# Optimization experiments

Hardware: AMD Instinct MI355X
Metric: run time of the kernel (lower is better)

The kernel has to match this reference:

```python
import jax, jax.numpy as jnp
import numpy as np

LN_EPS = 1e-6

def layernorm(x, w, b):
    m = jnp.mean(x, axis=-1, keepdims=True)
    v = jnp.mean((x - m) ** 2, axis=-1, keepdims=True)
    return (x - m) * jax.lax.rsqrt(v + LN_EPS) * w + b

def rotate_half(x):
    x1, x2 = jnp.split(x, 2, axis=-1)
    return jnp.concatenate([-x2, x1], axis=-1)

def headwise_lowrank(x, U, V, b):
    # x: [B,S,D], U: [H,D,r], V: [H,r,hd] -> [B,S,H*hd]
    xu = jnp.einsum('bsd,hdr->bshr', x, U)
    y = jnp.einsum('bshr,hre->bshe', xu, V)
    B, S, H, E = y.shape
    return y.reshape(B, S, H * E) + b

def setup_inputs() -> dict:
    key = jax.random.key(0)
    B, S, D, H, HD = 4, 2048, 768, 12, 64
    RA, RF, DFF = 32, 512, 3072
    ks = jax.random.split(key, 20)
    s = 0.02
    inp = {
        'x': jax.random.normal(ks[0], (B, S, D), jnp.float32),
        'attn_norm_w': jnp.ones((D,), jnp.float32),
        'attn_norm_b': jnp.zeros((D,), jnp.float32),
        'Uq': jax.random.normal(ks[1], (H, D, RA), jnp.float32) * s,
        'Vq': jax.random.normal(ks[2], (H, RA, HD), jnp.float32),
        'bq': jax.random.normal(ks[3], (D,), jnp.float32) * s,
        'Uk': jax.random.normal(ks[4], (H, D, RA), jnp.float32) * s,
        'Vk': jax.random.normal(ks[5], (H, RA, HD), jnp.float32),
        'bk': jax.random.normal(ks[6], (D,), jnp.float32) * s,
        'Uv': jax.random.normal(ks[7], (H, D, RA), jnp.float32) * s,
        'Vv': jax.random.normal(ks[8], (H, RA, HD), jnp.float32),
        'bv': jax.random.normal(ks[9], (D,), jnp.float32) * s,
        'Wo_w': jax.random.normal(ks[10], (D, D), jnp.float32) * s,
        'Wo_b': jax.random.normal(ks[11], (D,), jnp.float32) * s,
        'mlp_norm_w': jnp.ones((D,), jnp.float32),
        'mlp_norm_b': jnp.zeros((D,), jnp.float32),
        'Ui': jax.random.normal(ks[12], (D, RF), jnp.float32) * s,
        'Vi': jax.random.normal(ks[13], (RF, 2 * DFF), jnp.float32),
        'bi': jax.random.normal(ks[14], (2 * DFF,), jnp.float32) * s,
        'Uo': jax.random.normal(ks[15], (DFF, RF), jnp.float32) * s,
        'Vo': jax.random.normal(ks[16], (RF, D), jnp.float32),
        'bo': jax.random.normal(ks[17], (D,), jnp.float32) * s,
    }
    # real RoPE tables [S, HD]
    inv_freq = 1.0 / (10000.0 ** (np.arange(0, HD, 2, dtype=np.float32) / HD))
    t = np.arange(S, dtype=np.float32)
    freqs = np.outer(t, inv_freq)  # [S, HD/2]
    emb = np.concatenate([freqs, freqs], axis=-1)
    inp['cos'] = jnp.asarray(np.cos(emb))
    inp['sin'] = jnp.asarray(np.sin(emb))
    return inp

def reference(x, attn_norm_w, attn_norm_b, Uq, Vq, bq, Uk, Vk, bk, Uv, Vv, bv,
              cos, sin, Wo_w, Wo_b, mlp_norm_w, mlp_norm_b, Ui, Vi, bi, Uo, Vo, bo):
    B, S, D = x.shape
    H, HD = Vq.shape[0], Vq.shape[2]
    # --- attention sub-block (pre-norm) ---
    h = layernorm(x, attn_norm_w, attn_norm_b)
    q = headwise_lowrank(h, Uq, Vq, bq).reshape(B, S, H, HD).transpose(0, 2, 1, 3)
    k = headwise_lowrank(h, Uk, Vk, bk).reshape(B, S, H, HD).transpose(0, 2, 1, 3)
    v = headwise_lowrank(h, Uv, Vv, bv).reshape(B, S, H, HD).transpose(0, 2, 1, 3)
    c = cos[None, None]  # [1,1,S,HD]
    s_ = sin[None, None]
    q = q * c + rotate_half(q) * s_
    k = k * c + rotate_half(k) * s_
    scale = 1.0 / jnp.sqrt(jnp.asarray(HD, q.dtype))
    scores = jnp.einsum('bhqd,bhkd->bhqk', q, k) * scale
    attn = jax.nn.softmax(scores, axis=-1)
    o = jnp.einsum('bhqk,bhkd->bhqd', attn, v)
    o = o.transpose(0, 2, 1, 3).reshape(B, S, D)
    x1 = x + o @ Wo_w.T + Wo_b
    # --- FFN sub-block (pre-norm, low-rank GEGLU) ---
    h2 = layernorm(x1, mlp_norm_w, mlp_norm_b)
    u = (h2 @ Ui) @ Vi + bi  # [B,S,2*dff]
    g1, g2 = jnp.split(u, 2, axis=-1)
    g = jax.nn.gelu(g1, approximate=True) * g2
    y = (g @ Uo) @ Vo + bo
    return x1 + y
```

## Files before the change

kernel.cpp:

```cpp
#include <hip/hip_runtime.h>
#include <hip/hip_bf16.h>
#include <math.h>

#define NTOK 8192
#define SEQ  2048
#define DM   768
#define NH   12
#define HD2  64
#define RA   32
#define NG   3072

typedef __attribute__((ext_vector_type(8))) short bf16x8;
typedef __attribute__((ext_vector_type(4))) float f32x4;

__device__ __forceinline__ float b2f(unsigned short u) {
    union { unsigned int i; float f; } v; v.i = ((unsigned int)u) << 16; return v.f;
}
__device__ __forceinline__ unsigned short f2b_rne(float f) {
    union { float f; unsigned int i; } v; v.f = f;
    unsigned int b = v.i + 0x7FFFu + ((v.i >> 16) & 1u);
    return (unsigned short)(b >> 16);
}
__device__ __forceinline__ float wval(const void* p, size_t i, int bf) {
    return bf ? b2f(((const unsigned short*)p)[i]) : ((const float*)p)[i];
}
__device__ __forceinline__ unsigned int cvt_pk_bf16(float a, float b) {
    unsigned int r;
    asm("v_cvt_pk_bf16_f32 %0, %1, %2" : "=v"(r) : "v"(a), "v"(b));
    return r;
}

__global__ void detect_kernel(const unsigned int* __restrict__ w1, int* __restrict__ flag) {
    *flag = (w1[0] == 0x3F800000u) ? 0 : 1;
}

__global__ __launch_bounds__(256) void conv_f32_kernel(const void* __restrict__ src,
        float* __restrict__ dst, int n, const int* __restrict__ flag) {
    int i = blockIdx.x * 256 + threadIdx.x;
    if (i < n)
        dst[i] = (*flag) ? b2f(((const unsigned short*)src)[i]) : ((const float*)src)[i];
}

__global__ __launch_bounds__(256) void conv_b16_kernel(const void* __restrict__ src,
        unsigned short* __restrict__ dst, int n, const int* __restrict__ flag) {
    int i = blockIdx.x * 256 + threadIdx.x;
    if (i < n)
        dst[i] = (*flag) ? ((const unsigned short*)src)[i] : f2b_rne(((const float*)src)[i]);
}

__global__ __launch_bounds__(256) void conv_split_kernel(const void* __restrict__ src,
        unsigned short* __restrict__ hi, unsigned short* __restrict__ lo,
        int n, const int* __restrict__ flag) {
    int i = blockIdx.x * 256 + threadIdx.x;
    if (i < n) {
        float v = (*flag) ? b2f(((const unsigned short*)src)[i]) : ((const float*)src)[i];
        unsigned short h = f2b_rne(v);
        hi[i] = h;
        lo[i] = f2b_rne(v - b2f(h));
    }
}

__global__ __launch_bounds__(256) void ln_kernel(const float* __restrict__ x,
        const void* __restrict__ w, const void* __restrict__ b,
        void* __restrict__ out, void* __restrict__ out2,
        const int* __restrict__ flag, int mode) {
    int bf = *flag;
    int row = blockIdx.x, tid = threadIdx.x;
    const float* xr = x + (size_t)row * DM;
    float v0 = xr[tid];
    float v1 = xr[tid + 256];
    float v2 = xr[tid + 512];
    float s = v0 + v1 + v2;
    float ss = v0 * v0 + v1 * v1 + v2 * v2;
    #pragma unroll
    for (int off = 32; off >= 1; off >>= 1) {
        s  += __shfl_xor(s, off);
        ss += __shfl_xor(ss, off);
    }
    __shared__ float rs[4], rq[4];
    int wid = tid >> 6;
    if ((tid & 63) == 0) { rs[wid] = s; rq[wid] = ss; }
    __syncthreads();
    s  = rs[0] + rs[1] + rs[2] + rs[3];
    ss = rq[0] + rq[1] + rq[2] + rq[3];
    float mean = s * (1.0f / DM);
    float var  = ss * (1.0f / DM) - mean * mean;
    float inv  = rsqrtf(var + 1e-6f);
    float o0 = (v0 - mean) * inv * wval(w, tid, bf)       + wval(b, tid, bf);
    float o1 = (v1 - mean) * inv * wval(w, tid + 256, bf) + wval(b, tid + 256, bf);
    float o2 = (v2 - mean) * inv * wval(w, tid + 512, bf) + wval(b, tid + 512, bf);
    if (mode == 2) {
        unsigned short* oh = (unsigned short*)out  + (size_t)row * DM;
        unsigned short* ol = (unsigned short*)out2 + (size_t)row * DM;
        unsigned short h0 = f2b_rne(o0), h1 = f2b_rne(o1), h2 = f2b_rne(o2);
        oh[tid] = h0; oh[tid + 256] = h1; oh[tid + 512] = h2;
        ol[tid]       = f2b_rne(o0 - b2f(h0));
        ol[tid + 256] = f2b_rne(o1 - b2f(h1));
        ol[tid + 512] = f2b_rne(o2 - b2f(h2));
    } else if (mode == 1) {
        unsigned short* orow = (unsigned short*)out + (size_t)row * DM;
        orow[tid] = f2b_rne(o0); orow[tid + 256] = f2b_rne(o1); orow[tid + 512] = f2b_rne(o2);
    } else {
        float* orow = (float*)out + (size_t)row * DM;
        orow[tid] = o0; orow[tid + 256] = o1; orow[tid + 512] = o2;
    }
}

__global__ __launch_bounds__(256) void xu_mfma(
        const unsigned short* __restrict__ Ah, const unsigned short* __restrict__ Al,
        const unsigned short* __restrict__ Uh0, const unsigned short* __restrict__ Ul0,
        const unsigned short* __restrict__ Uh1, const unsigned short* __restrict__ Ul1,
        const unsigned short* __restrict__ Uh2, const unsigned short* __restrict__ Ul2,
        float* __restrict__ XU) {
    __shared__ unsigned short Ash[128][40], Asl[128][40];
    __shared__ unsigned short Bsh[128][40], Bsl[128][40];
    int tid = threadIdx.x;
    int w = tid >> 6, lane = tid & 63;
    int n16 = lane & 15, quad = lane >> 4;
    int m0 = blockIdx.x * 128, n0 = blockIdx.y * 128;
    int which = n0 / 384;
    const unsigned short* Uh = (which == 0) ? Uh0 : (which == 1) ? Uh1 : Uh2;
    const unsigned short* Ul = (which == 0) ? Ul0 : (which == 1) ? Ul1 : Ul2;
    int nh0 = n0 - which * 384;
    int mh = (w & 1) * 64, nh = (w >> 1) * 64;
    f32x4 acc[4][4] = {};

    int am = tid >> 1, akb = (tid & 1) * 16;
    const unsigned short* ahp = Ah + (size_t)(m0 + am) * DM + akb;
    const unsigned short* alp = Al + (size_t)(m0 + am) * DM + akb;
    int kp = (tid & 15) * 2, nb = (tid >> 4) * 8;
    int hc = nh0 + nb;
    int head = hc >> 5, rr = hc & 31;
    size_t bbase = (size_t)head * (DM * RA) + (size_t)kp * RA + rr;

    uint4 rah0 = *(const uint4*)ahp,       rah1 = *(const uint4*)(ahp + 8);
    uint4 ral0 = *(const uint4*)alp,       ral1 = *(const uint4*)(alp + 8);
    uint4 rbh0 = *(const uint4*)(Uh + bbase);
    uint4 rbh1 = *(const uint4*)(Uh + bbase + RA);
    uint4 rbl0 = *(const uint4*)(Ul + bbase);
    uint4 rbl1 = *(const uint4*)(Ul + bbase + RA);

    for (int k0 = 0; k0 < DM; k0 += 32) {
        __builtin_amdgcn_s_barrier();
        *(uint4*)&Ash[am][akb]     = rah0;
        *(uint4*)&Ash[am][akb + 8] = rah1;
        *(uint4*)&Asl[am][akb]     = ral0;
        *(uint4*)&Asl[am][akb + 8] = ral1;
        {
            const unsigned int* a = (const unsigned int*)&rbh0;
            const unsigned int* b = (const unsigned int*)&rbh1;
            #pragma unroll
            for (int d = 0; d < 4; d++) {
                *(unsigned int*)&Bsh[nb + 2 * d][kp]     = (a[d] & 0xFFFFu) | (b[d] << 16);
                *(unsigned int*)&Bsh[nb + 2 * d + 1][kp] = (a[d] >> 16) | (b[d] & 0xFFFF0000u);
            }
            const unsigned int* c = (const unsigned int*)&rbl0;
            const unsigned int* e = (const unsigned int*)&rbl1;
            #pragma unroll
            for (int d = 0; d < 4; d++) {
                *(unsigned int*)&Bsl[nb + 2 * d][kp]     = (c[d] & 0xFFFFu) | (e[d] << 16);
                *(unsigned int*)&Bsl[nb + 2 * d + 1][kp] = (c[d] >> 16) | (e[d] & 0xFFFF0000u);
            }
        }
        if (k0 + 32 < DM) {
            rah0 = *(const uint4*)(ahp + k0 + 32); rah1 = *(const uint4*)(ahp + k0 + 40);
            ral0 = *(const uint4*)(alp + k0 + 32); ral1 = *(const uint4*)(alp + k0 + 40);
            size_t nbb = bbase + (size_t)(k0 + 32) * RA;
            rbh0 = *(const uint4*)(Uh + nbb); rbh1 = *(const uint4*)(Uh + nbb + RA);
            rbl0 = *(const uint4*)(Ul + nbb); rbl1 = *(const uint4*)(Ul + nbb + RA);
        }
        asm volatile("s_waitcnt lgkmcnt(0)" ::: "memory");
        __builtin_amdgcn_s_barrier();
        bf16x8 ah[4], al[4], bh[4], bl[4];
        #pragma unroll
        for (int i = 0; i < 4; i++) {
            ah[i] = *(const bf16x8*)&Ash[mh + i * 16 + n16][quad * 8];
            al[i] = *(const bf16x8*)&Asl[mh + i * 16 + n16][quad * 8];
            bh[i] = *(const bf16x8*)&Bsh[nh + i * 16 + n16][quad * 8];
            bl[i] = *(const bf16x8*)&Bsl[nh + i * 16 + n16][quad * 8];
        }
        #pragma unroll
        for (int mi = 0; mi < 4; mi++)
            #pragma unroll
            for (int ni = 0; ni < 4; ni++) {
                acc[mi][ni] = __builtin_amdgcn_mfma_f32_16x16x32_bf16(ah[mi], bh[ni], acc[mi][ni], 0, 0, 0);
                acc[mi][ni] = __builtin_amdgcn_mfma_f32_16x16x32_bf16(ah[mi], bl[ni], acc[mi][ni], 0, 0, 0);
                acc[mi][ni] = __builtin_amdgcn_mfma_f32_16x16x32_bf16(al[mi], bh[ni], acc[mi][ni], 0, 0, 0);
            }
    }
    #pragma unroll
    for (int mi = 0; mi < 4; mi++)
        #pragma unroll
        for (int ni = 0; ni < 4; ni++) {
            int col = n0 + nh + ni * 16 + n16;
            #pragma unroll
            for (int r = 0; r < 4; r++) {
                int row = m0 + mh + mi * 16 + quad * 4 + r;
                XU[(size_t)row * 1152 + col] = acc[mi][ni][r];
            }
        }
}

__global__ __launch_bounds__(256) void qkv2_kernel(
        const float* __restrict__ XU,
        const void* __restrict__ Vq, const void* __restrict__ bq,
        const void* __restrict__ Vk, const void* __restrict__ bk,
        const void* __restrict__ Vv, const void* __restrict__ bv,
        const void* __restrict__ cosT, const void* __restrict__ sinT,
        unsigned short* __restrict__ qhg, unsigned short* __restrict__ qlg,
        unsigned short* __restrict__ khg, unsigned short* __restrict__ klg,
        unsigned short* __restrict__ vtg, const int* __restrict__ flag) {
    int bf = *flag;
    int tok0 = blockIdx.x * 64;
    int head = blockIdx.y;
    int tid = threadIdx.x;
    int row = tid >> 2;
    int e0  = (tid & 3) * 16;
    int tok = tok0 + row;
    int bb = tok >> 11, ssp = tok & (SEQ - 1);
    int ssp0 = tok0 & (SEQ - 1);
    int bh = bb * NH + head;
    __shared__ float XUs[64][33];
    __shared__ float Vws[32][65];
    __shared__ float obs[64][65];
    const void* Vp[3] = {Vq, Vk, Vv};
    const void* bp[3] = {bq, bk, bv};
    for (int which = 0; which < 3; which++) {
        __syncthreads();
        for (int i = tid; i < 2048; i += 256) {
            int rr = i >> 5, r = i & 31;
            XUs[rr][r] = XU[(size_t)(tok0 + rr) * 1152 + which * 384 + head * 32 + r];
        }
        for (int i = tid; i < 2048; i += 256) {
            int r = i >> 6, e = i & 63;
            Vws[r][e] = wval(Vp[which], (size_t)head * RA * HD2 + (size_t)r * 64 + e, bf);
        }
        __syncthreads();
        float acc[16];
        #pragma unroll
        for (int j = 0; j < 16; j++) acc[j] = wval(bp[which], head * 64 + e0 + j, bf);
        #pragma unroll 8
        for (int r = 0; r < 32; r++) {
            float xv = XUs[row][r];
            #pragma unroll
            for (int j = 0; j < 16; j++) acc[j] += xv * Vws[r][e0 + j];
        }
        #pragma unroll
        for (int j = 0; j < 16; j++) obs[row][e0 + j] = acc[j];
        __syncthreads();
        if (which == 2) {
            int e = tid >> 2, seg = (tid & 3) * 16;
            unsigned short buf[16];
            #pragma unroll
            for (int i = 0; i < 16; i++) buf[i] = f2b_rne(obs[seg + i][e]);
            unsigned short* dp = vtg + ((size_t)bh * 64 + e) * SEQ + ssp0 + seg;
            *(uint4*)dp = ((const uint4*)buf)[0];
            *(uint4*)(dp + 8) = ((const uint4*)buf)[1];
        } else {
            float scale = (which == 0) ? 0.18033688011112042f : 1.0f;
            unsigned short hbuf[16], lbuf[16];
            #pragma unroll
            for (int j = 0; j < 16; j++) {
                int e = e0 + j;
                float c  = wval(cosT, (size_t)ssp * 64 + e, bf);
                float sn = wval(sinT, (size_t)ssp * 64 + e, bf);
                float other = (e < 32) ? -obs[row][e + 32] : obs[row][e - 32];
                float val = (acc[j] * c + other * sn) * scale;
                unsigned short h = f2b_rne(val);
                hbuf[j] = h;
                lbuf[j] = f2b_rne(val - b2f(h));
            }
            unsigned short* hp = ((which == 0) ? qhg : khg) + ((size_t)bh * SEQ + ssp) * 64 + e0;
            unsigned short* lp = ((which == 0) ? qlg : klg) + ((size_t)bh * SEQ + ssp) * 64 + e0;
            *(uint4*)hp = ((const uint4*)hbuf)[0];
            *(uint4*)(hp + 8) = ((const uint4*)hbuf)[1];
            *(uint4*)lp = ((const uint4*)lbuf)[0];
            *(uint4*)(lp + 8) = ((const uint4*)lbuf)[1];
        }
    }
}

__global__ __launch_bounds__(256) void attn_mfma(
        const unsigned short* __restrict__ qh, const unsigned short* __restrict__ ql,
        const unsigned short* __restrict__ kh, const unsigned short* __restrict__ kl,
        const unsigned short* __restrict__ vt, unsigned short* __restrict__ og) {
    int qt = blockIdx.x, bh = blockIdx.y;
    int bb = bh / NH, hh = bh - bb * NH;
    int tid = threadIdx.x;
    int w = tid >> 6, lane = tid & 63;
    int n16 = lane & 15, quad = lane >> 4;

    __shared__ __align__(16) unsigned short Khs[64][64];
    __shared__ __align__(16) unsigned short Kls[64][64];
    __shared__ __align__(16) unsigned short VTs[64][64];
    __shared__ __align__(16) unsigned short Pbs[4][16][64];

    size_t qoff = ((size_t)bh * SEQ + qt * 64 + w * 16 + n16) * 64 + quad * 8;
    bf16x8 aqh0 = *(const bf16x8*)(qh + qoff);
    bf16x8 aqh1 = *(const bf16x8*)(qh + qoff + 32);
    bf16x8 aql0 = *(const bf16x8*)(ql + qoff);
    bf16x8 aql1 = *(const bf16x8*)(ql + qoff + 32);

    bf16x8 vones;
    #pragma unroll
    for (int i = 0; i < 8; i++) vones[i] = (short)0x3F80;

    float m[4] = {-1e30f, -1e30f, -1e30f, -1e30f};
    float l[4] = {0.f, 0.f, 0.f, 0.f};
    f32x4 O[4] = {};
    const unsigned short* kh_p = kh + (size_t)bh * SEQ * 64;
    const unsigned short* kl_p = kl + (size_t)bh * SEQ * 64;
    const unsigned short* vt_p = vt + (size_t)bh * 64 * SEQ;

    int row0 = tid >> 3, ch = tid & 7;
    int row1 = row0 + 32;
    int sw0 = (ch ^ (row0 & 7)) * 8;
    int sw1 = (ch ^ (row1 & 7)) * 8;
    size_t ko0 = (size_t)row0 * 64 + ch * 8;
    size_t ko1 = (size_t)row1 * 64 + ch * 8;
    size_t vo0 = (size_t)row0 * SEQ + ch * 8;
    size_t vo1 = (size_t)row1 * SEQ + ch * 8;

    uint4 rkh0 = *(const uint4*)(kh_p + ko0);
    uint4 rkh1 = *(const uint4*)(kh_p + ko1);
    uint4 rkl0 = *(const uint4*)(kl_p + ko0);
    uint4 rkl1 = *(const uint4*)(kl_p + ko1);
    uint4 rv0  = *(const uint4*)(vt_p + vo0);
    uint4 rv1  = *(const uint4*)(vt_p + vo1);

    int px = n16 & 7;
    int c0 = (quad ^ px) * 8;
    int c1 = ((quad + 4) ^ px) * 8;

    for (int t0 = 0; t0 < SEQ; t0 += 64) {
        __builtin_amdgcn_s_barrier();
        *(uint4*)&Khs[row0][sw0] = rkh0;
        *(uint4*)&Khs[row1][sw1] = rkh1;
        *(uint4*)&Kls[row0][sw0] = rkl0;
        *(uint4*)&Kls[row1][sw1] = rkl1;
        *(uint4*)&VTs[row0][sw0] = rv0;
        *(uint4*)&VTs[row1][sw1] = rv1;
        if (t0 + 64 < SEQ) {
            size_t kt = (size_t)(t0 + 64) * 64;
            rkh0 = *(const uint4*)(kh_p + kt + ko0);
            rkh1 = *(const uint4*)(kh_p + kt + ko1);
            rkl0 = *(const uint4*)(kl_p + kt + ko0);
            rkl1 = *(const uint4*)(kl_p + kt + ko1);
            rv0  = *(const uint4*)(vt_p + (t0 + 64) + vo0);
            rv1  = *(const uint4*)(vt_p + (t0 + 64) + vo1);
        }
        asm volatile("s_waitcnt lgkmcnt(0)" ::: "memory");
        __builtin_amdgcn_s_barrier();

        f32x4 s[4];
        #pragma unroll
        for (int t = 0; t < 4; t++) {
            int rr = 16 * t + n16;
            bf16x8 bkh0 = *(const bf16x8*)&Khs[rr][c0];
            bf16x8 bkh1 = *(const bf16x8*)&Khs[rr][c1];
            bf16x8 bkl0 = *(const bf16x8*)&Kls[rr][c0];
            bf16x8 bkl1 = *(const bf16x8*)&Kls[rr][c1];
            f32x4 a = {};
            a = __builtin_amdgcn_mfma_f32_16x16x32_bf16(aqh0, bkh0, a, 0, 0, 0);
            a = __builtin_amdgcn_mfma_f32_16x16x32_bf16(aqh1, bkh1, a, 0, 0, 0);
            a = __builtin_amdgcn_mfma_f32_16x16x32_bf16(aqh0, bkl0, a, 0, 0, 0);
            a = __builtin_amdgcn_mfma_f32_16x16x32_bf16(aqh1, bkl1, a, 0, 0, 0);
            a = __builtin_amdgcn_mfma_f32_16x16x32_bf16(aql0, bkh0, a, 0, 0, 0);
            a = __builtin_amdgcn_mfma_f32_16x16x32_bf16(aql1, bkh1, a, 0, 0, 0);
            s[t] = a;
        }
        float mt[4];
        #pragma unroll
        for (int r = 0; r < 4; r++) {
            float v = fmaxf(fmaxf(s[0][r], s[1][r]), fmaxf(s[2][r], s[3][r]));
            v = fmaxf(v, __shfl_xor(v, 1));
            v = fmaxf(v, __shfl_xor(v, 2));
            v = fmaxf(v, __shfl_xor(v, 4));
            v = fmaxf(v, __shfl_xor(v, 8));
            mt[r] = v;
        }
        float need = fmaxf(fmaxf(mt[0] - m[0], mt[1] - m[1]),
                           fmaxf(mt[2] - m[2], mt[3] - m[3]));
        if (__any(need > 8.0f)) {
            #pragma unroll
            for (int r = 0; r < 4; r++) {
                float mn = fmaxf(m[r], mt[r]);
                float al = exp2f(m[r] - mn);
                m[r] = mn;
                l[r] *= al;
                #pragma unroll
                for (int t2 = 0; t2 < 4; t2++) O[t2][r] *= al;
            }
        }
        int qr = quad * 4;
        #pragma unroll
        for (int t = 0; t < 4; t++) {
            float p0 = exp2f(s[t][0] - m[0]);
            float p1 = exp2f(s[t][1] - m[1]);
            float p2 = exp2f(s[t][2] - m[2]);
            float p3 = exp2f(s[t][3] - m[3]);
            unsigned int pk01 = cvt_pk_bf16(p0, p1);
            unsigned int pk23 = cvt_pk_bf16(p2, p3);
            int cb = 2 * t + (n16 >> 3);
            Pbs[w][qr + 0][((cb ^ ((qr + 0) & 7)) << 3) | px] = (unsigned short)pk01;
            Pbs[w][qr + 1][((cb ^ ((qr + 1) & 7)) << 3) | px] = (unsigned short)(pk01 >> 16);
            Pbs[w][qr + 2][((cb ^ ((qr + 2) & 7)) << 3) | px] = (unsigned short)pk23;
            Pbs[w][qr + 3][((cb ^ ((qr + 3) & 7)) << 3) | px] = (unsigned short)(pk23 >> 16);
        }
        bf16x8 ap0 = *(const bf16x8*)&Pbs[w][n16][c0];
        bf16x8 ap1 = *(const bf16x8*)&Pbs[w][n16][c1];
        f32x4 ls = {};
        ls = __builtin_amdgcn_mfma_f32_16x16x32_bf16(ap0, vones, ls, 0, 0, 0);
        ls = __builtin_amdgcn_mfma_f32_16x16x32_bf16(ap1, vones, ls, 0, 0, 0);
        #pragma unroll
        for (int r = 0; r < 4; r++) l[r] += ls[r];
        #pragma unroll
        for (int t2 = 0; t2 < 4; t2++) {
            bf16x8 bv0 = *(const bf16x8*)&VTs[16 * t2 + n16][c0];
            bf16x8 bv1 = *(const bf16x8*)&VTs[16 * t2 + n16][c1];
            O[t2] = __builtin_amdgcn_mfma_f32_16x16x32_bf16(ap0, bv0, O[t2], 0, 0, 0);
            O[t2] = __builtin_amdgcn_mfma_f32_16x16x32_bf16(ap1, bv1, O[t2], 0, 0, 0);
        }
    }
    int srow = qt * 64 + w * 16 + quad * 4;
    #pragma unroll
    for (int r = 0; r < 4; r++) {
        float inv = 1.0f / l[r];
        unsigned short* op = og + ((size_t)bb * SEQ + srow + r) * DM + hh * HD2 + n16;
        #pragma unroll
        for (int t2 = 0; t2 < 4; t2++)
            op[16 * t2] = f2b_rne(O[t2][r] * inv);
    }
}

template <int MODE, bool TB>
__global__ __launch_bounds__(512) void gemm_bf16(
        const unsigned short* __restrict__ A, const unsigned short* __restrict__ Bw,
        const void* __restrict__ bias, const float* __restrict__ resid,
        void* __restrict__ Cout, int Nn, int K, const int* __restrict__ flag) {
    __shared__ unsigned short As[128][40];
    __shared__ unsigned short Bs[128][40];
    int tid = threadIdx.x;
    int w = tid >> 6, lane = tid & 63;
    int n16 = lane & 15, quad = lane >> 4;
    int m0 = blockIdx.x * 128, n0 = blockIdx.y * 128;
    int mh = (w & 3) * 32, nh = (w >> 2) * 64;
    f32x4 acc[2][4] = {};

    int st = tid & 255;
    bool isA = tid < 256;
    int am = st >> 1, akb = (st & 1) * 16;
    int bkp = (st & 15) * 2, bnb = (st >> 4) * 8;
    int bn = st >> 1, bkb = (st & 1) * 16;
    const unsigned short* gp0;
    const unsigned short* gp1;
    if (isA) {
        gp0 = A + (size_t)(m0 + am) * K + akb;
        gp1 = gp0 + 8;
    } else if (!TB) {
        gp0 = Bw + (size_t)bkp * Nn + n0 + bnb;
        gp1 = gp0 + Nn;
    } else {
        gp0 = Bw + (size_t)(n0 + bn) * K + bkb;
        gp1 = gp0 + 8;
    }
    uint4 r0 = *(const uint4*)gp0;
    uint4 r1 = *(const uint4*)gp1;

    for (int k0 = 0; k0 < K; k0 += 32) {
        __builtin_amdgcn_s_barrier();
        if (isA) {
            *(uint4*)&As[am][akb]     = r0;
            *(uint4*)&As[am][akb + 8] = r1;
        } else if (!TB) {
            const unsigned int* a = (const unsigned int*)&r0;
            const unsigned int* b = (const unsigned int*)&r1;
            #pragma unroll
            for (int d = 0; d < 4; d++) {
                *(unsigned int*)&Bs[bnb + 2 * d][bkp]     = (a[d] & 0xFFFFu) | (b[d] << 16);
                *(unsigned int*)&Bs[bnb + 2 * d + 1][bkp] = (a[d] >> 16) | (b[d] & 0xFFFF0000u);
            }
        } else {
            *(uint4*)&Bs[bn][bkb]     = r0;
            *(uint4*)&Bs[bn][bkb + 8] = r1;
        }
        if (k0 + 32 < K) {
            size_t adv = (isA || TB) ? (size_t)(k0 + 32) : (size_t)(k0 + 32) * Nn;
            r0 = *(const uint4*)(gp0 + adv);
            r1 = *(const uint4*)(gp1 + adv);
        }
        asm volatile("s_waitcnt lgkmcnt(0)" ::: "memory");
        __builtin_amdgcn_s_barrier();
        bf16x8 af[2], bfr[4];
        #pragma unroll
        for (int i = 0; i < 2; i++)
            af[i] = *(const bf16x8*)&As[mh + i * 16 + n16][quad * 8];
        #pragma unroll
        for (int i = 0; i < 4; i++)
            bfr[i] = *(const bf16x8*)&Bs[nh + i * 16 + n16][quad * 8];
        #pragma unroll
        for (int mi = 0; mi < 2; mi++)
            #pragma unroll
            for (int ni = 0; ni < 4; ni++)
                acc[mi][ni] = __builtin_amdgcn_mfma_f32_16x16x32_bf16(af[mi], bfr[ni], acc[mi][ni], 0, 0, 0);
    }
    int bf = (MODE == 0) ? 0 : *flag;
    #pragma unroll
    for (int ni = 0; ni < 4; ni++) {
        int col = n0 + nh + ni * 16 + n16;
        float bv = (MODE == 0) ? 0.f : wval(bias, col, bf);
        #pragma unroll
        for (int mi = 0; mi < 2; mi++) {
            #pragma unroll
            for (int r = 0; r < 4; r++) {
                int row = m0 + mh + mi * 16 + quad * 4 + r;
                float val = acc[mi][ni][r];
                if constexpr (MODE == 0) {
                    ((unsigned short*)Cout)[(size_t)row * Nn + col] = f2b_rne(val);
                } else if constexpr (MODE == 1) {
                    ((float*)Cout)[(size_t)row * Nn + col] =
                        val + bv + resid[(size_t)row * Nn + col];
                } else {
                    float o = val + bv + resid[(size_t)row * Nn + col];
                    if (bf)
                        ((unsigned short*)Cout)[(size_t)row * Nn + col] = f2b_rne(o);
                    else
                        ((float*)Cout)[(size_t)row * Nn + col] = o;
                }
            }
        }
    }
}

__global__ __launch_bounds__(256) void geglu_bf16(
        const unsigned short* __restrict__ A, const unsigned short* __restrict__ Bw,
        const void* __restrict__ bias, unsigned short* __restrict__ G,
        const int* __restrict__ flag) {
    int bf = *flag;
    const int K = 512, Nn = 2 * NG;
    __shared__ unsigned short As[128][40];
    __shared__ unsigned short B1s[64][40];
    __shared__ unsigned short B2s[64][40];
    int tid = threadIdx.x;
    int w = tid >> 6, lane = tid & 63;
    int n16 = lane & 15, quad = lane >> 4;
    int m0 = blockIdx.x * 128, n0 = blockIdx.y * 64;
    int mh = (w & 1) * 64;
    int nq = (w >> 1) * 32;
    f32x4 acc1[4][2] = {}, acc2[4][2] = {};

    int am = tid >> 1, akb = (tid & 1) * 16;
    const unsigned short* aptr = A + (size_t)(m0 + am) * K + akb;
    uint4 ra0 = *(const uint4*)aptr;
    uint4 ra1 = *(const uint4*)(aptr + 8);
    int t_ = tid & 127, hsel = tid >> 7;
    int bkp = (t_ & 15) * 2, bnb = (t_ >> 4) * 8;
    const unsigned short* bptr = Bw + (size_t)bkp * Nn + n0 + (size_t)hsel * NG + bnb;
    uint4 rb0 = *(const uint4*)bptr;
    uint4 rb1 = *(const uint4*)(bptr + Nn);

    for (int k0 = 0; k0 < K; k0 += 32) {
        __builtin_amdgcn_s_barrier();
        *(uint4*)&As[am][akb]     = ra0;
        *(uint4*)&As[am][akb + 8] = ra1;
        {
            const unsigned int* a = (const unsigned int*)&rb0;
            const unsigned int* b = (const unsigned int*)&rb1;
            unsigned short (*Bst)[40] = hsel ? B2s : B1s;
            #pragma unroll
            for (int d = 0; d < 4; d++) {
                *(unsigned int*)&Bst[bnb + 2 * d][bkp]     = (a[d] & 0xFFFFu) | (b[d] << 16);
                *(unsigned int*)&Bst[bnb + 2 * d + 1][bkp] = (a[d] >> 16) | (b[d] & 0xFFFF0000u);
            }
        }
        if (k0 + 32 < K) {
            ra0 = *(const uint4*)(aptr + k0 + 32);
            ra1 = *(const uint4*)(aptr + k0 + 40);
            const unsigned short* nbp = bptr + (size_t)(k0 + 32) * Nn;
            rb0 = *(const uint4*)nbp;
            rb1 = *(const uint4*)(nbp + Nn);
        }
        asm volatile("s_waitcnt lgkmcnt(0)" ::: "memory");
        __builtin_amdgcn_s_barrier();
        bf16x8 af[4], b1f[2], b2f_[2];
        #pragma unroll
        for (int i = 0; i < 4; i++)
            af[i] = *(const bf16x8*)&As[mh + i * 16 + n16][quad * 8];
        #pragma unroll
        for (int i = 0; i < 2; i++) {
            b1f[i]  = *(const bf16x8*)&B1s[nq + i * 16 + n16][quad * 8];
            b2f_[i] = *(const bf16x8*)&B2s[nq + i * 16 + n16][quad * 8];
        }
        #pragma unroll
        for (int mi = 0; mi < 4; mi++)
            #pragma unroll
            for (int ni = 0; ni < 2; ni++) {
                acc1[mi][ni] = __builtin_amdgcn_mfma_f32_16x16x32_bf16(af[mi], b1f[ni], acc1[mi][ni], 0, 0, 0);
                acc2[mi][ni] = __builtin_amdgcn_mfma_f32_16x16x32_bf16(af[mi], b2f_[ni], acc2[mi][ni], 0, 0, 0);
            }
    }
    #pragma unroll
    for (int ni = 0; ni < 2; ni++) {
        int ccol = nq + ni * 16 + n16;
        float b1 = wval(bias, n0 + ccol, bf);
        float b2 = wval(bias, NG + n0 + ccol, bf);
        #pragma unroll
        for (int mi = 0; mi < 4; mi++) {
            #pragma unroll
            for (int r = 0; r < 4; r++) {
                int rrow = mh + mi * 16 + quad * 4 + r;
                float u1 = acc1[mi][ni][r] + b1;
                float u2 = acc2[mi][ni][r] + b2;
                float nz = fminf(-2.3022083f * (u1 + 0.044715f * u1 * u1 * u1), 126.f);
                float gl = u1 * __builtin_amdgcn_rcpf(1.0f + exp2f(nz));
                G[(size_t)(m0 + rrow) * NG + n0 + ccol] = f2b_rne(gl * u2);
            }
        }
    }
}

extern "C" void kernel_launch(void* const* d_in, const int* in_sizes, int n_in,
                              void* d_out, int out_size, void* d_ws, size_t ws_size,
                              hipStream_t stream) {
    (void)in_sizes; (void)n_in; (void)out_size; (void)ws_size;
    const size_t ND = (size_t)NTOK * DM;
    const int USZ = NH * DM * RA;

    float* ws = (float*)d_ws;
    int*   flag = (int*)d_ws;
    float* xf = ws + 256;
    float* P0 = xf + ND;
    float* P1 = P0 + ND;
    float* P2 = P1 + ND;
    float* P3 = P2 + ND;
    float* P4 = P3 + ND;
    float* P5 = P4 + ND;
    float* XU = P4;

    unsigned short* hH = (unsigned short*)P0;
    unsigned short* hL = hH + ND;
    unsigned short* qhb = (unsigned short*)P1;
    unsigned short* qlb = qhb + ND;
    unsigned short* khb = qhb + 2 * ND;
    unsigned short* klb = qhb + 3 * ND;
    unsigned short* vtb = qhb + 4 * ND;
    unsigned short* ob  = (unsigned short*)P0;
    unsigned short* h2b = (unsigned short*)P1;
    unsigned short* tb  = (unsigned short*)P2;
    unsigned short* gb  = (unsigned short*)P3;
    unsigned short* t2b = (unsigned short*)P0;
    unsigned short* wb  = (unsigned short*)(P5 + ND);
    unsigned short* WoB = wb;
    unsigned short* UiB = WoB + 589824;
    unsigned short* ViB = UiB + 393216;
    unsigned short* UoB = ViB + 3145728;
    unsigned short* VoB = UoB + 1572864;
    unsigned short* UqH = VoB + 393216;
    unsigned short* UqL = UqH + USZ;
    unsigned short* UkH = UqL + USZ;
    unsigned short* UkL = UkH + USZ;
    unsigned short* UvH = UkL + USZ;
    unsigned short* UvL = UvH + USZ;

    detect_kernel<<<1, 1, 0, stream>>>((const unsigned int*)d_in[1], flag);
    conv_f32_kernel<<<(int)((ND + 255) / 256), 256, 0, stream>>>(d_in[0], xf, (int)ND, flag);
    conv_b16_kernel<<<(589824 + 255) / 256, 256, 0, stream>>>(d_in[12], WoB, 589824, flag);
    conv_b16_kernel<<<(393216 + 255) / 256, 256, 0, stream>>>(d_in[16], UiB, 393216, flag);
    conv_b16_kernel<<<(3145728 + 255) / 256, 256, 0, stream>>>(d_in[17], ViB, 3145728, flag);
    conv_b16_kernel<<<(1572864 + 255) / 256, 256, 0, stream>>>(d_in[19], UoB, 1572864, flag);
    conv_b16_kernel<<<(393216 + 255) / 256, 256, 0, stream>>>(d_in[20], VoB, 393216, flag);
    conv_split_kernel<<<(USZ + 255) / 256, 256, 0, stream>>>(d_in[3], UqH, UqL, USZ, flag);
    conv_split_kernel<<<(USZ + 255) / 256, 256, 0, stream>>>(d_in[6], UkH, UkL, USZ, flag);
    conv_split_kernel<<<(USZ + 255) / 256, 256, 0, stream>>>(d_in[9], UvH, UvL, USZ, flag);

    ln_kernel<<<NTOK, 256, 0, stream>>>(xf, d_in[1], d_in[2], hH, hL, flag, 2);
    xu_mfma<<<dim3(64, 9), 256, 0, stream>>>(hH, hL, UqH, UqL, UkH, UkL, UvH, UvL, XU);
    qkv2_kernel<<<dim3(NTOK / 64, NH), 256, 0, stream>>>(XU,
                                         d_in[4], d_in[5], d_in[7], d_in[8],
                                         d_in[10], d_in[11], d_in[22], d_in[23],
                                         qhb, qlb, khb, klb, vtb, flag);
    attn_mfma<<<dim3(SEQ / 64, 4 * NH), 256, 0, stream>>>(qhb, qlb, khb, klb, vtb, ob);
    gemm_bf16<1, true><<<dim3(64, 6), 512, 0, stream>>>(ob, WoB, d_in[13], xf,
                                                        (void*)P5, DM, DM, flag);
    ln_kernel<<<NTOK, 256, 0, stream>>>(P5, d_in[14], d_in[15], (void*)h2b, nullptr, flag, 1);
    gemm_bf16<0, false><<<dim3(64, 4), 512, 0, stream>>>(h2b, UiB, nullptr, nullptr,
                                                         (void*)tb, 512, DM, flag);
    geglu_bf16<<<dim3(64, 48), 256, 0, stream>>>(tb, ViB, d_in[18], gb, flag);
    gemm_bf16<0, false><<<dim3(64, 4), 512, 0, stream>>>(gb, UoB, nullptr, nullptr,
                                                         (void*)t2b, 512, NG, flag);
    gemm_bf16<3, false><<<dim3(64, 6), 512, 0, stream>>>(t2b, VoB, d_in[21], P5,
                                                         d_out, DM, 512, flag);
}
```

Baseline: 740.2 us.

## Drop bf16 hi/lo split for Q/K in attention, use single bf16 and transposed scores

Q and K are now stored as a single bf16 value instead of a hi/lo bf16 pair, so the score computation uses 2 MFMAs per tile instead of 6, and the K low-part LDS buffer and its global loads are removed. The score MFMA operands are swapped so each lane holds one query column, which lets the running max be a single scalar per lane reduced with two shuffles instead of four per-row reductions. P stores become vectorized uint2 writes through precomputed swizzled pointers. This cuts matrix work and memory traffic in the attention kernel at the cost of lower precision in the QK^T scores.

```diff
diff --git a/kernel.cpp b/kernel.cpp
--- a/kernel.cpp
+++ b/kernel.cpp
@@ -207,8 +207,7 @@
         const void* __restrict__ Vk, const void* __restrict__ bk,
         const void* __restrict__ Vv, const void* __restrict__ bv,
         const void* __restrict__ cosT, const void* __restrict__ sinT,
-        unsigned short* __restrict__ qhg, unsigned short* __restrict__ qlg,
-        unsigned short* __restrict__ khg, unsigned short* __restrict__ klg,
+        unsigned short* __restrict__ qg, unsigned short* __restrict__ kg,
         unsigned short* __restrict__ vtg, const int* __restrict__ flag) {
     int bf = *flag;
     int tok0 = blockIdx.x * 64;
@@ -258,7 +257,7 @@
             *(uint4*)(dp + 8) = ((const uint4*)buf)[1];
         } else {
             float scale = (which == 0) ? 0.18033688011112042f : 1.0f;
-            unsigned short hbuf[16], lbuf[16];
+            unsigned short hbuf[16];
             #pragma unroll
             for (int j = 0; j < 16; j++) {
                 int e = e0 + j;
@@ -266,23 +265,17 @@
                 float sn = wval(sinT, (size_t)ssp * 64 + e, bf);
                 float other = (e < 32) ? -obs[row][e + 32] : obs[row][e - 32];
                 float val = (acc[j] * c + other * sn) * scale;
-                unsigned short h = f2b_rne(val);
-                hbuf[j] = h;
-                lbuf[j] = f2b_rne(val - b2f(h));
-            }
-            unsigned short* hp = ((which == 0) ? qhg : khg) + ((size_t)bh * SEQ + ssp) * 64 + e0;
-            unsigned short* lp = ((which == 0) ? qlg : klg) + ((size_t)bh * SEQ + ssp) * 64 + e0;
+                hbuf[j] = f2b_rne(val);
+            }
+            unsigned short* hp = ((which == 0) ? qg : kg) + ((size_t)bh * SEQ + ssp) * 64 + e0;
             *(uint4*)hp = ((const uint4*)hbuf)[0];
             *(uint4*)(hp + 8) = ((const uint4*)hbuf)[1];
-            *(uint4*)lp = ((const uint4*)lbuf)[0];
-            *(uint4*)(lp + 8) = ((const uint4*)lbuf)[1];
         }
     }
 }
 
 __global__ __launch_bounds__(256) void attn_mfma(
-        const unsigned short* __restrict__ qh, const unsigned short* __restrict__ ql,
-        const unsigned short* __restrict__ kh, const unsigned short* __restrict__ kl,
+        const unsigned short* __restrict__ qg, const unsigned short* __restrict__ kg,
         const unsigned short* __restrict__ vt, unsigned short* __restrict__ og) {
     int qt = blockIdx.x, bh = blockIdx.y;
     int bb = bh / NH, hh = bh - bb * NH;
@@ -291,25 +284,21 @@
     int n16 = lane & 15, quad = lane >> 4;
 
     __shared__ __align__(16) unsigned short Khs[64][64];
-    __shared__ __align__(16) unsigned short Kls[64][64];
     __shared__ __align__(16) unsigned short VTs[64][64];
     __shared__ __align__(16) unsigned short Pbs[4][16][64];
 
     size_t qoff = ((size_t)bh * SEQ + qt * 64 + w * 16 + n16) * 64 + quad * 8;
-    bf16x8 aqh0 = *(const bf16x8*)(qh + qoff);
-    bf16x8 aqh1 = *(const bf16x8*)(qh + qoff + 32);
-    bf16x8 aql0 = *(const bf16x8*)(ql + qoff);
-    bf16x8 aql1 = *(const bf16x8*)(ql + qoff + 32);
+    bf16x8 aq0 = *(const bf16x8*)(qg + qoff);
+    bf16x8 aq1 = *(const bf16x8*)(qg + qoff + 32);
 
     bf16x8 vones;
     #pragma unroll
     for (int i = 0; i < 8; i++) vones[i] = (short)0x3F80;
 
-    float m[4] = {-1e30f, -1e30f, -1e30f, -1e30f};
+    float mm = -1e30f;
     float l[4] = {0.f, 0.f, 0.f, 0.f};
     f32x4 O[4] = {};
-    const unsigned short* kh_p = kh + (size_t)bh * SEQ * 64;
-    const unsigned short* kl_p = kl + (size_t)bh * SEQ * 64;
+    const unsigned short* k_p  = kg + (size_t)bh * SEQ * 64;
     const unsigned short* vt_p = vt + (size_t)bh * 64 * SEQ;
 
     int row0 = tid >> 3, ch = tid & 7;
@@ -321,33 +310,31 @@
     size_t vo0 = (size_t)row0 * SEQ + ch * 8;
     size_t vo1 = (size_t)row1 * SEQ + ch * 8;
 
-    uint4 rkh0 = *(const uint4*)(kh_p + ko0);
-    uint4 rkh1 = *(const uint4*)(kh_p + ko1);
-    uint4 rkl0 = *(const uint4*)(kl_p + ko0);
-    uint4 rkl1 = *(const uint4*)(kl_p + ko1);
-    uint4 rv0  = *(const uint4*)(vt_p + vo0);
-    uint4 rv1  = *(const uint4*)(vt_p + vo1);
+    uint4 rk0 = *(const uint4*)(k_p + ko0);
+    uint4 rk1 = *(const uint4*)(k_p + ko1);
+    uint4 rv0 = *(const uint4*)(vt_p + vo0);
+    uint4 rv1 = *(const uint4*)(vt_p + vo1);
 
     int px = n16 & 7;
     int c0 = (quad ^ px) * 8;
     int c1 = ((quad + 4) ^ px) * 8;
+    unsigned short* pst[4];
+    #pragma unroll
+    for (int t = 0; t < 4; t++)
+        pst[t] = &Pbs[w][n16][(((2 * t + (quad >> 1)) ^ px) << 3) + ((quad & 1) << 2)];
 
     for (int t0 = 0; t0 < SEQ; t0 += 64) {
         __builtin_amdgcn_s_barrier();
-        *(uint4*)&Khs[row0][sw0] = rkh0;
-        *(uint4*)&Khs[row1][sw1] = rkh1;
-        *(uint4*)&Kls[row0][sw0] = rkl0;
-        *(uint4*)&Kls[row1][sw1] = rkl1;
+        *(uint4*)&Khs[row0][sw0] = rk0;
+        *(uint4*)&Khs[row1][sw1] = rk1;
         *(uint4*)&VTs[row0][sw0] = rv0;
         *(uint4*)&VTs[row1][sw1] = rv1;
         if (t0 + 64 < SEQ) {
             size_t kt = (size_t)(t0 + 64) * 64;
-            rkh0 = *(const uint4*)(kh_p + kt + ko0);
-            rkh1 = *(const uint4*)(kh_p + kt + ko1);
-            rkl0 = *(const uint4*)(kl_p + kt + ko0);
-            rkl1 = *(const uint4*)(kl_p + kt + ko1);
-            rv0  = *(const uint4*)(vt_p + (t0 + 64) + vo0);
-            rv1  = *(const uint4*)(vt_p + (t0 + 64) + vo1);
+            rk0 = *(const uint4*)(k_p + kt + ko0);
+            rk1 = *(const uint4*)(k_p + kt + ko1);
+            rv0 = *(const uint4*)(vt_p + (t0 + 64) + vo0);
+            rv1 = *(const uint4*)(vt_p + (t0 + 64) + vo1);
         }
         asm volatile("s_waitcnt lgkmcnt(0)" ::: "memory");
         __builtin_amdgcn_s_barrier();
@@ -356,56 +343,37 @@
         #pragma unroll
         for (int t = 0; t < 4; t++) {
             int rr = 16 * t + n16;
-            bf16x8 bkh0 = *(const bf16x8*)&Khs[rr][c0];
-            bf16x8 bkh1 = *(const bf16x8*)&Khs[rr][c1];
-            bf16x8 bkl0 = *(const bf16x8*)&Kls[rr][c0];
-            bf16x8 bkl1 = *(const bf16x8*)&Kls[rr][c1];
+            bf16x8 bk0 = *(const bf16x8*)&Khs[rr][c0];
+            bf16x8 bk1 = *(const bf16x8*)&Khs[rr][c1];
             f32x4 a = {};
-            a = __builtin_amdgcn_mfma_f32_16x16x32_bf16(aqh0, bkh0, a, 0, 0, 0);
-            a = __builtin_amdgcn_mfma_f32_16x16x32_bf16(aqh1, bkh1, a, 0, 0, 0);
-            a = __builtin_amdgcn_mfma_f32_16x16x32_bf16(aqh0, bkl0, a, 0, 0, 0);
-            a = __builtin_amdgcn_mfma_f32_16x16x32_bf16(aqh1, bkl1, a, 0, 0, 0);
-            a = __builtin_amdgcn_mfma_f32_16x16x32_bf16(aql0, bkh0, a, 0, 0, 0);
-            a = __builtin_amdgcn_mfma_f32_16x16x32_bf16(aql1, bkh1, a, 0, 0, 0);
+            a = __builtin_amdgcn_mfma_f32_16x16x32_bf16(bk0, aq0, a, 0, 0, 0);
+            a = __builtin_amdgcn_mfma_f32_16x16x32_bf16(bk1, aq1, a, 0, 0, 0);
             s[t] = a;
         }
-        float mt[4];
-        #pragma unroll
-        for (int r = 0; r < 4; r++) {
-            float v = fmaxf(fmaxf(s[0][r], s[1][r]), fmaxf(s[2][r], s[3][r]));
-            v = fmaxf(v, __shfl_xor(v, 1));
-            v = fmaxf(v, __shfl_xor(v, 2));
-            v = fmaxf(v, __shfl_xor(v, 4));
-            v = fmaxf(v, __shfl_xor(v, 8));
-            mt[r] = v;
-        }
-        float need = fmaxf(fmaxf(mt[0] - m[0], mt[1] - m[1]),
-                           fmaxf(mt[2] - m[2], mt[3] - m[3]));
-        if (__any(need > 8.0f)) {
+        float smax = fmaxf(fmaxf(s[0][0], s[0][1]), fmaxf(s[0][2], s[0][3]));
+        #pragma unroll
+        for (int t = 1; t < 4; t++)
+            smax = fmaxf(smax, fmaxf(fmaxf(s[t][0], s[t][1]), fmaxf(s[t][2], s[t][3])));
+        smax = fmaxf(smax, __shfl_xor(smax, 16));
+        smax = fmaxf(smax, __shfl_xor(smax, 32));
+        if (__any(smax - mm > 8.0f)) {
+            float mn = fmaxf(mm, smax);
+            float al = exp2f(mm - mn);
+            mm = mn;
             #pragma unroll
             for (int r = 0; r < 4; r++) {
-                float mn = fmaxf(m[r], mt[r]);
-                float al = exp2f(m[r] - mn);
-                m[r] = mn;
-                l[r] *= al;
+                float ar = __shfl(al, quad * 4 + r);
+                l[r] *= ar;
                 #pragma unroll
-                for (int t2 = 0; t2 < 4; t2++) O[t2][r] *= al;
-            }
-        }
-        int qr = quad * 4;
+                for (int t2 = 0; t2 < 4; t2++) O[t2][r] *= ar;
+            }
+        }
         #pragma unroll
         for (int t = 0; t < 4; t++) {
-            float p0 = exp2f(s[t][0] - m[0]);
-            float p1 = exp2f(s[t][1] - m[1]);
-            float p2 = exp2f(s[t][2] - m[2]);
-            float p3 = exp2f(s[t][3] - m[3]);
-            unsigned int pk01 = cvt_pk_bf16(p0, p1);
-            unsigned int pk23 = cvt_pk_bf16(p2, p3);
-            int cb = 2 * t + (n16 >> 3);
-            Pbs[w][qr + 0][((cb ^ ((qr + 0) & 7)) << 3) | px] = (unsigned short)pk01;
-            Pbs[w][qr + 1][((cb ^ ((qr + 1) & 7)) << 3) | px] = (unsigned short)(pk01 >> 16);
-            Pbs[w][qr + 2][((cb ^ ((qr + 2) & 7)) << 3) | px] = (unsigned short)pk23;
-            Pbs[w][qr + 3][((cb ^ ((qr + 3) & 7)) << 3) | px] = (unsigned short)(pk23 >> 16);
+            unsigned int pk01 = cvt_pk_bf16(exp2f(s[t][0] - mm), exp2f(s[t][1] - mm));
+            unsigned int pk23 = cvt_pk_bf16(exp2f(s[t][2] - mm), exp2f(s[t][3] - mm));
+            uint2 pv; pv.x = pk01; pv.y = pk23;
+            *(uint2*)pst[t] = pv;
         }
         bf16x8 ap0 = *(const bf16x8*)&Pbs[w][n16][c0];
         bf16x8 ap1 = *(const bf16x8*)&Pbs[w][n16][c1];
@@ -639,11 +607,9 @@
 
     unsigned short* hH = (unsigned short*)P0;
     unsigned short* hL = hH + ND;
-    unsigned short* qhb = (unsigned short*)P1;
-    unsigned short* qlb = qhb + ND;
-    unsigned short* khb = qhb + 2 * ND;
-    unsigned short* klb = qhb + 3 * ND;
-    unsigned short* vtb = qhb + 4 * ND;
+    unsigned short* qb  = (unsigned short*)P1;
+    unsigned short* kb  = qb + ND;
+    unsigned short* vtb = qb + 2 * ND;
     unsigned short* ob  = (unsigned short*)P0;
     unsigned short* h2b = (unsigned short*)P1;
     unsigned short* tb  = (unsigned short*)P2;
@@ -678,8 +644,8 @@
     qkv2_kernel<<<dim3(NTOK / 64, NH), 256, 0, stream>>>(XU,
                                          d_in[4], d_in[5], d_in[7], d_in[8],
                                          d_in[10], d_in[11], d_in[22], d_in[23],
-                                         qhb, qlb, khb, klb, vtb, flag);
-    attn_mfma<<<dim3(SEQ / 64, 4 * NH), 256, 0, stream>>>(qhb, qlb, khb, klb, vtb, ob);
+                                         qb, kb, vtb, flag);
+    attn_mfma<<<dim3(SEQ / 64, 4 * NH), 256, 0, stream>>>(qb, kb, vtb, ob);
     gemm_bf16<1, true><<<dim3(64, 6), 512, 0, stream>>>(ob, WoB, d_in[13], xf,
                                                         (void*)P5, DM, DM, flag);
     ln_kernel<<<NTOK, 256, 0, stream>>>(P5, d_in[14], d_in[15], (void*)h2b, nullptr, flag, 1);
```

Result: faster. 686.5 us (-7.3%).
